# Optimization experiments

Hardware: AMD Instinct MI355X
Metric: run time of the kernel (lower is better)

Reference implementation:

```python
import jax, jax.numpy as jnp
import numpy as np

N_NODES = 50000
N_EDGES = 800000
IN_F = 128
OUT_F = 32
HEADS = 4
EDGE_DIM = 8
ALPHA = 0.2  # LeakyReLU negative slope


def setup_inputs() -> dict:
    key = jax.random.key(0)
    k0, k1, k2, k3, k4 = jax.random.split(key, 5)
    x = jax.random.normal(k0, (N_NODES, IN_F), dtype=jnp.float32)
    edge_index = jax.random.randint(k1, (2, N_EDGES), 0, N_NODES, dtype=jnp.int32)
    edge_attr = jax.random.normal(k2, (N_EDGES, EDGE_DIM), dtype=jnp.float32)
    # xavier-ish init for parameters
    W = jax.random.normal(k3, (HEADS, IN_F, OUT_F), dtype=jnp.float32) * (1.0 / np.float32(np.sqrt(IN_F)))
    a = jax.random.normal(k4, (HEADS, 2 * OUT_F + EDGE_DIM, 1), dtype=jnp.float32) * np.float32(0.1)
    return {"x": x, "edge_index": edge_index, "edge_attr": edge_attr, "W": W, "a": a}


def reference(x, edge_index, edge_attr, W, a):
    n_nodes = x.shape[0]
    out_f = W.shape[2]
    src, dst = edge_index[0], edge_index[1]

    # per-head linear transform: (N, H, O)
    xt = jnp.einsum('ni,hio->nho', x, W)
    x_src = xt[src]  # (E, H, O) edge gather
    x_dst = xt[dst]  # (E, H, O)

    # split attention vector a = [a_src | a_dst | a_edge]; equivalent to
    # einsum('ehi,hio->eho', cat([x_src, x_dst, edge]), a) without the concat
    av = a[..., 0]                      # (H, 2O+D)
    a_s = av[:, :out_f]                 # (H, O)
    a_d = av[:, out_f:2 * out_f]        # (H, O)
    a_e = av[:, 2 * out_f:]             # (H, D)
    e = (jnp.einsum('eho,ho->eh', x_src, a_s)
         + jnp.einsum('eho,ho->eh', x_dst, a_d)
         + edge_attr @ a_e.T)           # (E, H)
    e = jnp.where(e > 0, e, ALPHA * e)  # LeakyReLU

    # segment (per-destination) softmax over incoming edges, per head
    max_e = jax.ops.segment_max(e, dst, num_segments=n_nodes)   # (N, H), -inf on empty
    max_e = jnp.where(jnp.isneginf(max_e), jnp.zeros_like(max_e), max_e)
    exp_e = jnp.exp(e - max_e[dst])                             # (E, H)
    sum_exp = jax.ops.segment_sum(exp_e, dst, num_segments=n_nodes)  # (N, H)
    attention = exp_e / (sum_exp[dst] + 1e-10)                  # (E, H)

    # weighted scatter-add aggregation
    weighted = x_src * attention[:, :, None]                    # (E, H, O)
    out = jax.ops.segment_sum(weighted, dst, num_segments=n_nodes)  # (N, H, O)
    return out.reshape(n_nodes, -1)  # concat=True -> (N, H*O)
```

## Files before the change

### kernel.cpp

```cpp
#include <hip/hip_runtime.h>
#include <hip/hip_fp16.h>

#define N_NODES 50000
#define N_EDGES 800000
#define IN_F    128
#define OUT_F   32
#define HEADS   4
#define EDGE_DIM 8
#define LRELU_ALPHA 0.2f

#define EPB 2048
#define BT  1024
#define EPT (EPB / BT)
#define NBUCK 98
#define NBLK_A ((N_EDGES + EPB - 1) / EPB)
#define NODES_PER_BUCK 512
#define CAP 10240

typedef float    floatx4 __attribute__((ext_vector_type(4)));
typedef unsigned uintx4  __attribute__((ext_vector_type(4)));
typedef short    short4v __attribute__((ext_vector_type(4)));
typedef short    short8v __attribute__((ext_vector_type(8)));
typedef float    f32x4   __attribute__((ext_vector_type(4)));

__device__ __forceinline__ unsigned f2bf(float f) {
  unsigned u = __float_as_uint(f);
  return (u + 0x7fffu + ((u >> 16) & 1u)) >> 16;
}

__global__ __launch_bounds__(256) void k_transform(
    const float* __restrict__ x, const float* __restrict__ W,
    unsigned* __restrict__ xtb, unsigned* __restrict__ bfill) {
  __shared__ short sxb[64][138];
  __shared__ short wt[128][138];
  const int t = threadIdx.x;
  const int n0 = blockIdx.x * 64;

  if (blockIdx.x == 0 && t < NBUCK) bfill[t] = (unsigned)(t * CAP);

#pragma unroll
  for (int r = 0; r < 64; ++r) {
    const int idx = r * 256 + t;
    const int h = idx >> 12;
    const int i = (idx >> 5) & 127;
    const int o = idx & 31;
    wt[h * 32 + o][i] = (short)f2bf(W[idx]);
  }

#pragma unroll
  for (int r = 0; r < 8; ++r) {
    const int f = r * 256 + t;
    const int node = f >> 5;
    const int i4 = (f & 31) * 4;
    const int n = n0 + node;
    float4 v = make_float4(0.f, 0.f, 0.f, 0.f);
    if (n < N_NODES) v = *reinterpret_cast<const float4*>(&x[(size_t)n * 128 + i4]);
    short4v s4;
    s4.x = (short)f2bf(v.x);
    s4.y = (short)f2bf(v.y);
    s4.z = (short)f2bf(v.z);
    s4.w = (short)f2bf(v.w);
    *reinterpret_cast<short4v*>(&sxb[node][i4]) = s4;
  }
  __syncthreads();

  const int w = t >> 6;
  const int lane = t & 63;
  const int r16 = lane & 15;
  const int kg = lane >> 4;

  f32x4 acc[8];
#pragma unroll
  for (int nt = 0; nt < 8; ++nt) acc[nt] = (f32x4)(0.f);

#pragma unroll
  for (int kk = 0; kk < 4; ++kk) {
    const short8v afrag =
        *reinterpret_cast<const short8v*>(&sxb[w * 16 + r16][kk * 32 + kg * 8]);
#pragma unroll
    for (int nt = 0; nt < 8; ++nt) {
      const short8v bfrag =
          *reinterpret_cast<const short8v*>(&wt[nt * 16 + r16][kk * 32 + kg * 8]);
      acc[nt] = __builtin_amdgcn_mfma_f32_16x16x32_bf16(afrag, bfrag, acc[nt],
                                                        0, 0, 0);
    }
  }

#pragma unroll
  for (int nt = 0; nt < 8; ++nt) {
#pragma unroll
    for (int reg = 0; reg < 4; ++reg) {
      const float v = acc[nt][reg];
      const float vp = __shfl_xor(v, 1, 64);
      if (!(lane & 1)) {
        const int node = n0 + w * 16 + kg * 4 + reg;
        if (node < N_NODES) {
          const unsigned u = f2bf(v) | (f2bf(vp) << 16);
          xtb[(size_t)node * 64 + nt * 8 + (r16 >> 1)] = u;
        }
      }
    }
  }
}

__global__ __launch_bounds__(256) void k_alpha(
    const unsigned* __restrict__ xtb, const float* __restrict__ a,
    float* __restrict__ alpha_src, float* __restrict__ alpha_dst) {
  const int t = threadIdx.x;
  const int node = blockIdx.x * 64 + (t >> 2);
  if (node >= N_NODES) return;
  const int q = t & 3;
  const unsigned* __restrict__ row = &xtb[(size_t)node * 64 + q * 16];
  const float* __restrict__ as = &a[q * 72];
  const float* __restrict__ ad = &a[q * 72 + 32];
  float s = 0.f, d = 0.f;
#pragma unroll
  for (int j = 0; j < 16; ++j) {
    const unsigned u = row[j];
    const float lo = __uint_as_float(u << 16);
    const float hi = __uint_as_float(u & 0xffff0000u);
    s = fmaf(lo, as[2 * j], s);
    s = fmaf(hi, as[2 * j + 1], s);
    d = fmaf(lo, ad[2 * j], d);
    d = fmaf(hi, ad[2 * j + 1], d);
  }
  alpha_src[node * 4 + q] = s;
  alpha_dst[node * 4 + q] = d;
}

__device__ __forceinline__ uintx4 make_entry(
    int e, int src, int dst, const float* __restrict__ ea,
    const float* __restrict__ a, const float* __restrict__ alpha_src,
    const float* __restrict__ alpha_dst) {
  const floatx4 ev0 = __builtin_nontemporal_load(
      reinterpret_cast<const floatx4*>(&ea[(size_t)e * EDGE_DIM]));
  const floatx4 ev1 = __builtin_nontemporal_load(
      reinterpret_cast<const floatx4*>(&ea[(size_t)e * EDGE_DIM + 4]));
  const float4 als = *reinterpret_cast<const float4*>(&alpha_src[src * 4]);
  const float4 ald = *reinterpret_cast<const float4*>(&alpha_dst[dst * 4]);
  const float* alsp = reinterpret_cast<const float*>(&als);
  const float* aldp = reinterpret_cast<const float*>(&ald);
  unsigned sh[4];
#pragma unroll
  for (int h = 0; h < HEADS; ++h) {
    float s = alsp[h] + aldp[h];
    const float* ae = &a[h * 72 + 64];
    s = fmaf(ev0.x, ae[0], s);
    s = fmaf(ev0.y, ae[1], s);
    s = fmaf(ev0.z, ae[2], s);
    s = fmaf(ev0.w, ae[3], s);
    s = fmaf(ev1.x, ae[4], s);
    s = fmaf(ev1.y, ae[5], s);
    s = fmaf(ev1.z, ae[6], s);
    s = fmaf(ev1.w, ae[7], s);
    s = s > 0.f ? s : LRELU_ALPHA * s;
    sh[h] = (unsigned)__half_as_ushort(__float2half(s));
  }
  uintx4 ent;
  ent.x = (unsigned)src;
  ent.y = sh[0] | (sh[1] << 16);
  ent.z = sh[2] | (sh[3] << 16);
  ent.w = (unsigned)dst;
  return ent;
}

__global__ __launch_bounds__(BT) void k_binsort(
    const int* __restrict__ ei, const float* __restrict__ ea,
    const float* __restrict__ a, const float* __restrict__ alpha_src,
    const float* __restrict__ alpha_dst, unsigned* __restrict__ bfill,
    uintx4* __restrict__ stage) {
  __shared__ uintx4 sent[EPB];
  __shared__ unsigned lhist[128];
  __shared__ unsigned lscan[128];
  __shared__ unsigned gb[128];
  const int t = threadIdx.x;
  const int e0 = blockIdx.x * EPB;
  const int nvalid = min(EPB, N_EDGES - e0);

  if (t < 128) lhist[t] = 0u;
  __syncthreads();

  uintx4 ent[EPT];
  int bk[EPT];
  int lpos[EPT];
#pragma unroll
  for (int k = 0; k < EPT; ++k) {
    const int e = e0 + k * BT + t;
    bk[k] = -1;
    if (e < N_EDGES) {
      const int src = __builtin_nontemporal_load(&ei[e]);
      const int dst = __builtin_nontemporal_load(&ei[N_EDGES + e]);
      ent[k] = make_entry(e, src, dst, ea, a, alpha_src, alpha_dst);
      bk[k] = dst >> 9;
      lpos[k] = (int)atomicAdd(&lhist[bk[k]], 1u);
    }
  }
  __syncthreads();

  if (t < 128) lscan[t] = lhist[t];
  __syncthreads();
#pragma unroll
  for (int off = 1; off < 128; off <<= 1) {
    unsigned v = 0u;
    if (t < 128 && t >= off) v = lscan[t - off];
    __syncthreads();
    if (t < 128) lscan[t] += v;
    __syncthreads();
  }
  if (t < NBUCK) {
    const unsigned cnt = lhist[t];
    lscan[t] -= cnt;
    gb[t] = cnt ? atomicAdd(&bfill[t], cnt) : 0u;
  }
  __syncthreads();

#pragma unroll
  for (int k = 0; k < EPT; ++k) {
    if (bk[k] >= 0) {
      const int p = (int)lscan[bk[k]] + lpos[k];
      sent[p] = ent[k];
    }
  }
  __syncthreads();

#pragma unroll
  for (int k = 0; k < EPT; ++k) {
    const int p = k * BT + t;
    if (p < nvalid) {
      const uintx4 sv = sent[p];
      const int b = (int)(sv.w >> 9);
      stage[gb[b] + (unsigned)(p - (int)lscan[b])] = sv;
    }
  }
}

__global__ __launch_bounds__(1024) void k_place(
    const unsigned* __restrict__ bfill, const uintx4* __restrict__ stage,
    unsigned* __restrict__ rs, uintx4* __restrict__ csr) {
  __shared__ unsigned lbuf[NODES_PER_BUCK];
  __shared__ unsigned wsum[8];
  __shared__ unsigned bscan[128];
  const int b = blockIdx.x;
  const int t = threadIdx.x;
  const int node0 = b << 9;
  const int nn = min(NODES_PER_BUCK, N_NODES - node0);
  const unsigned base = (unsigned)(b * CAP);

  if (t < 128) {
    bscan[t] = (t < NBUCK) ? (bfill[t] - (unsigned)(t * CAP)) : 0u;
  }
  __syncthreads();
#pragma unroll
  for (int off = 1; off < 128; off <<= 1) {
    unsigned v = 0u;
    if (t < 128 && t >= off) v = bscan[t - off];
    __syncthreads();
    if (t < 128) bscan[t] += v;
    __syncthreads();
  }
  const unsigned cnt = bfill[b] - base;
  const unsigned bs = (b == 0) ? 0u : bscan[b - 1];

  if (t < NODES_PER_BUCK) lbuf[t] = 0u;
  __syncthreads();

  for (unsigned i = t; i < cnt; i += 1024) {
    const unsigned dst = __builtin_nontemporal_load(&stage[base + i]).w;
    atomicAdd(&lbuf[dst - (unsigned)node0], 1u);
  }
  __syncthreads();

  const unsigned c = (t < NODES_PER_BUCK) ? lbuf[t] : 0u;
  unsigned incl = c;
  const int lane = t & 63;
#pragma unroll
  for (int off = 1; off < 64; off <<= 1) {
    const unsigned n = __shfl_up(incl, off, 64);
    if (lane >= off) incl += n;
  }
  if (t < NODES_PER_BUCK && lane == 63) wsum[t >> 6] = incl;
  __syncthreads();
  if (t < 8) {
    const unsigned wv = wsum[t];
    unsigned wincl = wv;
#pragma unroll
    for (int off = 1; off < 8; off <<= 1) {
      const unsigned n = __shfl_up(wincl, off, 64);
      if (t >= off) wincl += n;
    }
    wsum[t] = wincl - wv;
  }
  __syncthreads();
  if (t < NODES_PER_BUCK) {
    const unsigned excl = incl - c + wsum[t >> 6];
    lbuf[t] = bs + excl;
    if (t < nn) rs[node0 + t] = bs + excl;
  }
  if (b == NBUCK - 1 && t == 0) rs[N_NODES] = N_EDGES;
  __syncthreads();

  for (unsigned i = t; i < cnt; i += 1024) {
    const uintx4 ent = __builtin_nontemporal_load(&stage[base + i]);
    const unsigned slot = atomicAdd(&lbuf[ent.w - (unsigned)node0], 1u);
    csr[slot] = ent;
  }
}

__device__ __forceinline__ float ent_score(const uintx4& ent, int h) {
  const unsigned uu = (h < 2) ? ent.y : ent.z;
  const unsigned us = (h & 1) ? (uu >> 16) : (uu & 0xffffu);
  return __half2float(__ushort_as_half((unsigned short)us));
}

__global__ __launch_bounds__(256) void k_agg(
    const unsigned* __restrict__ rs, const uintx4* __restrict__ csr,
    const unsigned* __restrict__ xtb, float* __restrict__ out) {
  const int lane = threadIdx.x & 63;
  const int dst = (int)((blockIdx.x * (unsigned)blockDim.x + threadIdx.x) >> 6);
  if (dst >= N_NODES) return;

  const unsigned j0 = rs[dst];
  const unsigned j1 = rs[dst + 1];
  const int deg = (int)(j1 - j0);

  float a0 = 0.f, a1 = 0.f, lsum = 0.f;

  if (deg > 0) {
    const int rounds = (deg + 15) >> 4;
    const int eL = lane & 15;
    const int hB = lane >> 4;

    const uintx4 pad = {0u, 0xfc00fc00u, 0xfc00fc00u, 0u};

    for (int r = 0; r < rounds; ++r) {
      const int j = (int)j0 + r * 16 + eL;
      const uintx4 ent =
          (j < (int)j1) ? __builtin_nontemporal_load(&csr[j]) : pad;
      const float w = __expf(ent_score(ent, hB));
      lsum += w;
      const int sx = (int)ent.x;

      int ssrc[16];
#pragma unroll
      for (int jj = 0; jj < 16; ++jj)
        ssrc[jj] = __builtin_amdgcn_readlane(sx, jj);
      unsigned ud[16];
#pragma unroll
      for (int jj = 0; jj < 16; ++jj)
        ud[jj] = xtb[(size_t)ssrc[jj] * 64 + lane];
#define AGG_STEP(JJ)                                                         \
  {                                                                          \
    const float wj = __int_as_float(__builtin_amdgcn_ds_swizzle(             \
        __float_as_int(w), ((JJ) << 5) | 0x10));                             \
    a0 = fmaf(wj, __uint_as_float(ud[JJ] << 16), a0);                        \
    a1 = fmaf(wj, __uint_as_float(ud[JJ] & 0xffff0000u), a1);                \
  }
      AGG_STEP(0)  AGG_STEP(1)  AGG_STEP(2)  AGG_STEP(3)
      AGG_STEP(4)  AGG_STEP(5)  AGG_STEP(6)  AGG_STEP(7)
      AGG_STEP(8)  AGG_STEP(9)  AGG_STEP(10) AGG_STEP(11)
      AGG_STEP(12) AGG_STEP(13) AGG_STEP(14) AGG_STEP(15)
#undef AGG_STEP
    }
    lsum += __shfl_xor(lsum, 1, 64);
    lsum += __shfl_xor(lsum, 2, 64);
    lsum += __shfl_xor(lsum, 4, 64);
    lsum += __shfl_xor(lsum, 8, 64);
  }

  const float inv = 1.0f / (lsum + 1e-10f);
  __builtin_nontemporal_store(a0 * inv, &out[(size_t)dst * 128 + lane * 2 + 0]);
  __builtin_nontemporal_store(a1 * inv, &out[(size_t)dst * 128 + lane * 2 + 1]);
}

extern "C" void kernel_launch(void* const* d_in, const int* in_sizes, int n_in,
                              void* d_out, int out_size, void* d_ws,
                              size_t ws_size, hipStream_t stream) {
  const float* x = (const float*)d_in[0];
  const int* ei = (const int*)d_in[1];
  const float* ea = (const float*)d_in[2];
  const float* W = (const float*)d_in[3];
  const float* a = (const float*)d_in[4];
  float* out = (float*)d_out;

  char* p = (char*)d_ws;
  unsigned* xtb = (unsigned*)p;     p += (size_t)N_NODES * 64 * 4;
  uintx4* csr = (uintx4*)p;         p += (size_t)N_EDGES * 16;
  uintx4* stage = (uintx4*)p;       p += (size_t)NBUCK * CAP * 16;
  float* alpha_src = (float*)p;     p += (size_t)N_NODES * 4 * 4;
  float* alpha_dst = (float*)p;     p += (size_t)N_NODES * 4 * 4;
  unsigned* rs = (unsigned*)p;      p += (size_t)(N_NODES + 1) * 4;
  unsigned* bfill = (unsigned*)p;   p += 128 * 4;

  k_transform<<<(N_NODES + 63) / 64, 256, 0, stream>>>(x, W, xtb, bfill);
  k_alpha<<<(N_NODES + 63) / 64, 256, 0, stream>>>(xtb, a, alpha_src,
                                                   alpha_dst);
  k_binsort<<<NBLK_A, BT, 0, stream>>>(ei, ea, a, alpha_src, alpha_dst, bfill,
                                       stage);
  k_place<<<NBUCK, 1024, 0, stream>>>(bfill, stage, rs, csr);
  k_agg<<<(N_NODES * 64 + 255) / 256, 256, 0, stream>>>(rs, csr, xtb, out);
}
```

Baseline: 110.0 us.

## Precompute bf16 transposed W once and read it from global in transform

Adds a small k_wprep kernel that converts and transposes W to bf16 once, so each of the ~782 transform blocks no longer redoes the 16K-element conversion into shared memory. k_transform now uses 512 threads (8 waves), each wave computing 4 of the 8 output column tiles. B fragments are read from global/L2 instead of LDS, and the bfill init moves into the prep kernel. This removes redundant per-block work and cuts shared memory, which may raise occupancy. In exchange it adds one kernel launch and relies on L2 for the weight fragment reads.

Measured after the change: 117.0 us. +6.4%, slower.

```diff
diff --git a/kernel.cpp b/kernel.cpp
--- a/kernel.cpp
+++ b/kernel.cpp
@@ -28,28 +28,26 @@
   return (u + 0x7fffu + ((u >> 16) & 1u)) >> 16;
 }
 
-__global__ __launch_bounds__(256) void k_transform(
-    const float* __restrict__ x, const float* __restrict__ W,
-    unsigned* __restrict__ xtb, unsigned* __restrict__ bfill) {
+__global__ __launch_bounds__(128) void k_wprep(
+    const float* __restrict__ W, unsigned short* __restrict__ wtg,
+    unsigned* __restrict__ bfill) {
+  const int row = blockIdx.x;
+  const int i = threadIdx.x;
+  if (row == 0 && i < NBUCK) bfill[i] = (unsigned)(i * CAP);
+  const float v = W[(row >> 5) * (IN_F * OUT_F) + i * OUT_F + (row & 31)];
+  wtg[row * 128 + i] = (unsigned short)f2bf(v);
+}
+
+__global__ __launch_bounds__(512) void k_transform(
+    const float* __restrict__ x, const unsigned short* __restrict__ wtg,
+    unsigned* __restrict__ xtb) {
   __shared__ short sxb[64][138];
-  __shared__ short wt[128][138];
   const int t = threadIdx.x;
   const int n0 = blockIdx.x * 64;
 
-  if (blockIdx.x == 0 && t < NBUCK) bfill[t] = (unsigned)(t * CAP);
-
-#pragma unroll
-  for (int r = 0; r < 64; ++r) {
-    const int idx = r * 256 + t;
-    const int h = idx >> 12;
-    const int i = (idx >> 5) & 127;
-    const int o = idx & 31;
-    wt[h * 32 + o][i] = (short)f2bf(W[idx]);
-  }
-
-#pragma unroll
-  for (int r = 0; r < 8; ++r) {
-    const int f = r * 256 + t;
+#pragma unroll
+  for (int r = 0; r < 4; ++r) {
+    const int f = r * 512 + t;
     const int node = f >> 5;
     const int i4 = (f & 31) * 4;
     const int n = n0 + node;
@@ -65,38 +63,44 @@
   __syncthreads();
 
   const int w = t >> 6;
+  const int m = w & 3;
+  const int nt0 = (w >> 2) * 2;
   const int lane = t & 63;
   const int r16 = lane & 15;
   const int kg = lane >> 4;
 
-  f32x4 acc[8];
-#pragma unroll
-  for (int nt = 0; nt < 8; ++nt) acc[nt] = (f32x4)(0.f);
+  const int ntb = (w >> 2) * 4;
+
+  f32x4 acc[4];
+#pragma unroll
+  for (int q = 0; q < 4; ++q) acc[q] = (f32x4)(0.f);
 
 #pragma unroll
   for (int kk = 0; kk < 4; ++kk) {
+    const int koff = kk * 32 + kg * 8;
     const short8v afrag =
-        *reinterpret_cast<const short8v*>(&sxb[w * 16 + r16][kk * 32 + kg * 8]);
-#pragma unroll
-    for (int nt = 0; nt < 8; ++nt) {
-      const short8v bfrag =
-          *reinterpret_cast<const short8v*>(&wt[nt * 16 + r16][kk * 32 + kg * 8]);
-      acc[nt] = __builtin_amdgcn_mfma_f32_16x16x32_bf16(afrag, bfrag, acc[nt],
-                                                        0, 0, 0);
-    }
-  }
-
-#pragma unroll
-  for (int nt = 0; nt < 8; ++nt) {
+        *reinterpret_cast<const short8v*>(&sxb[m * 16 + r16][koff]);
+#pragma unroll
+    for (int q = 0; q < 4; ++q) {
+      const short8v bfrag = *reinterpret_cast<const short8v*>(
+          &wtg[((ntb + q) * 16 + r16) * 128 + koff]);
+      acc[q] = __builtin_amdgcn_mfma_f32_16x16x32_bf16(afrag, bfrag, acc[q],
+                                                       0, 0, 0);
+    }
+  }
+
+#pragma unroll
+  for (int q = 0; q < 4; ++q) {
+    const int nt = ntb + q;
 #pragma unroll
     for (int reg = 0; reg < 4; ++reg) {
-      const float v = acc[nt][reg];
+      const float v = acc[q][reg];
       const float vp = __shfl_xor(v, 1, 64);
       if (!(lane & 1)) {
-        const int node = n0 + w * 16 + kg * 4 + reg;
+        const int node = n0 + m * 16 + kg * 4 + reg;
         if (node < N_NODES) {
-          const unsigned u = f2bf(v) | (f2bf(vp) << 16);
-          xtb[(size_t)node * 64 + nt * 8 + (r16 >> 1)] = u;
+          xtb[(size_t)node * 64 + nt * 8 + (r16 >> 1)] =
+              f2bf(v) | (f2bf(vp) << 16);
         }
       }
     }
@@ -390,8 +394,10 @@
   float* alpha_dst = (float*)p;     p += (size_t)N_NODES * 4 * 4;
   unsigned* rs = (unsigned*)p;      p += (size_t)(N_NODES + 1) * 4;
   unsigned* bfill = (unsigned*)p;   p += 128 * 4;
-
-  k_transform<<<(N_NODES + 63) / 64, 256, 0, stream>>>(x, W, xtb, bfill);
+  unsigned short* wtg = (unsigned short*)p; p += 128 * 128 * 2;
+
+  k_wprep<<<128, 128, 0, stream>>>(W, wtg, bfill);
+  k_transform<<<(N_NODES + 63) / 64, 512, 0, stream>>>(x, wtg, xtb);
   k_alpha<<<(N_NODES + 63) / 64, 256, 0, stream>>>(xtb, a, alpha_src,
                                                    alpha_dst);
   k_binsort<<<NBLK_A, BT, 0, stream>>>(ei, ea, a, alpha_src, alpha_dst, bfill,
```
